# Optimization experiments

Hardware: AMD Instinct MI355X
Metric: run time of the kernel (lower is better)

Reference implementation:

```python
import jax, jax.numpy as jnp
import numpy as np

N = 1026; DX = 4096; DG = 4096; H0 = 4096; H1 = 2048; H2 = 1024
OUTS = 512; NL = 10; JH = 2048; E = 32832; K = 128; ALPHA = 0.05
INS = DX + DG  # 8192, edgeconv1 / joint_gemb input width

def _w(k, fan_in, shape):
    s = 1.0 / np.sqrt(fan_in)
    return jax.random.uniform(k, shape, minval=-s, maxval=s, dtype=jnp.float32)

def setup_inputs() -> dict:
    key = jax.random.key(0)
    ks = jax.random.split(key, 32)
    return dict(
        x=jax.random.normal(ks[0], (N, DX), jnp.float32),
        gx=jax.random.normal(ks[1], (N, DG), jnp.float32),
        edge_index=jax.random.randint(ks[2], (2, E), 0, N, dtype=jnp.int32),
        jw1=_w(ks[3], INS, (INS, JH)), jb1=_w(ks[4], INS, (JH,)),
        jw2=_w(ks[5], JH, (JH, N)), jb2=_w(ks[6], JH, (N,)),
        ec1_w=_w(ks[7], INS, (INS, H0)), ec1_b=_w(ks[8], INS, (H0,)),
        dr_w=_w(ks[9], H0, (H0, H2)), dr_b=_w(ks[10], H0, (H2,)),
        g1_w=_w(ks[11], H0, (H0, H1)), g1_b=_w(ks[12], H0, (H1,)),
        g2_w=_w(ks[13], H1, (H1, H2)), g2_b=_w(ks[14], H1, (H2,)),
        ec2_w=_w(ks[15], H2 + H1 + H0, (H2 + H1 + H0, H2)), ec2_b=_w(ks[16], H2 + H1 + H0, (H2,)),
        ec3_w=_w(ks[17], H2, (H2, OUTS)), ec3_b=_w(ks[18], H2, (OUTS,)),
        out_w=_w(ks[19], OUTS, (OUTS, NL)), out_b=_w(ks[20], OUTS, (NL,)),
    )

def _gdc(A):
    # GDC: self_loop_weight=1, sym norm in, exact PPR (alpha), topk(k, dim=0) sparsify, col norm out
    n = A.shape[0]
    eye = jnp.eye(n, dtype=A.dtype)
    A = A + eye  # self loops, weight 1
    deg = A.sum(axis=1)
    dinv = jax.lax.rsqrt(jnp.where(deg > 0, deg, 1.0))
    T = dinv[:, None] * A * dinv[None, :]          # D^-1/2 (A+I) D^-1/2
    S = ALPHA * jnp.linalg.inv(eye - (1.0 - ALPHA) * T)  # exact PPR diffusion
    vals, idx = jax.lax.top_k(S.T, K)              # top-K per column (dim=0)
    St = jnp.zeros((n, n), S.dtype).at[jnp.arange(n)[:, None], idx].set(vals)
    S = St.T
    csum = S.sum(axis=0)
    return S / jnp.where(csum == 0, 1.0, csum)[None, :]  # col normalization out

def _gcn(h_in, W, b, row, col, n):
    # PyG GCNConv: add self loops, sym-normalized aggregation, then bias
    h = h_in @ W
    deg = jax.ops.segment_sum(jnp.ones(row.shape[0], h.dtype), col, num_segments=n) + 1.0
    dinv = jax.lax.rsqrt(deg)
    agg = jax.ops.segment_sum(h[row] * (dinv[row] * dinv[col])[:, None], col, num_segments=n)
    return agg + h * (dinv * dinv)[:, None] + b

def _forward(x, gx, edge_index, jw1, jb1, jw2, jb2, ec1_w, ec1_b, dr_w, dr_b,
             g1_w, g1_b, g2_w, g2_b, ec2_w, ec2_b, ec3_w, ec3_b, out_w, out_b):
    row, col = edge_index[0], edge_index[1]
    xg = jnp.concatenate([x, gx], axis=1)                    # [N, INS]
    zz = jax.nn.relu(jax.nn.relu(xg @ jw1 + jb1) @ jw2 + jb2)  # joint_gemb -> [N, N] adjacency
    zz = _gdc(zz)
    xn = zz @ x                                              # nconv: dense neighbor aggregation
    z = jax.nn.relu(jnp.concatenate([xn, gx], axis=1) @ ec1_w + ec1_b)  # [N, H0]
    z0 = z @ dr_w + dr_b                                     # [N, H2]
    z1 = jax.nn.relu(_gcn(z + gx, g1_w, g1_b, row, col, N))  # [N, H1]
    z2 = jax.nn.relu(_gcn(z1, g2_w, g2_b, row, col, N))      # [N, H2]
    zc = jax.nn.relu(jnp.concatenate([z, z1, z2], axis=1) @ ec2_w + ec2_b)
    zf = jax.nn.relu((zc + z0) @ ec3_w + ec3_b)
    return zf @ out_w + out_b                                # [N, NL]

def reference(x, gx, edge_index, jw1, jb1, jw2, jb2, ec1_w, ec1_b, dr_w, dr_b,
              g1_w, g1_b, g2_w, g2_b, ec2_w, ec2_b, ec3_w, ec3_b, out_w, out_b):
    return _forward(x, gx, edge_index, jw1, jb1, jw2, jb2, ec1_w, ec1_b, dr_w, dr_b,
                    g1_w, g1_b, g2_w, g2_b, ec2_w, ec2_b, ec3_w, ec3_b, out_w, out_b)
```

## Files before the change

### kernel.cpp

```cpp
#include <hip/hip_runtime.h>
#include <stdint.h>

static constexpr int N_   = 1026;
static constexpr int DX_  = 4096;
static constexpr int DG_  = 4096;
static constexpr int H0_  = 4096;
static constexpr int H1_  = 2048;
static constexpr int H2_  = 1024;
static constexpr int OUTS_= 512;
static constexpr int NL_  = 10;
static constexpr int JH_  = 2048;
static constexpr int E_   = 32832;
static constexpr int K_   = 128;
static constexpr int INS_ = DX_ + DG_;
static constexpr int CAT2_= H0_ + H1_ + H2_;

static constexpr int MP_   = 1152;
static constexpr int KP1_  = 1056;

typedef _Float16 f16;
typedef __attribute__((ext_vector_type(8))) _Float16 f16x8;
typedef __attribute__((ext_vector_type(4))) _Float16 f16x4;
typedef __attribute__((ext_vector_type(4))) float    f32x4;

#define AS1C(p) ((const __attribute__((address_space(1))) unsigned int*)(p))
#define AS3(p)  ((__attribute__((address_space(3))) unsigned int*)(p))

__device__ __forceinline__ void gload16(const f16* g, f16* s) {
    __builtin_amdgcn_global_load_lds(AS1C(g), AS3(s), 16, 0, 0);
}

template<bool RELU, bool DUAL>
__global__ __launch_bounds__(512, DUAL ? 4 : 8)
void gemm_f16x2(int M, int Nc, int Kt, int chunkSteps,
                const f16* __restrict__ Ah, const f16* __restrict__ Al, int lda,
                const f16* __restrict__ Bh, const f16* __restrict__ Bl, int ldb,
                const float* __restrict__ bias, float alpha,
                const float* __restrict__ D, int ldd, float dscale,
                float* __restrict__ C, int ldc,
                f16* __restrict__ oAh, f16* __restrict__ oAl, int ldoa,
                f16* __restrict__ oBh, f16* __restrict__ oBl, int ldob,
                float* __restrict__ P, int Mp, int Ncp)
{
    __shared__ __align__(16) f16 sm[2][DUAL ? 4 : 2][4096];
    const int tid  = threadIdx.x;
    const int lane = tid & 63, w = tid >> 6;
    const int wr = w >> 1, wc = w & 1;
    const int bm = blockIdx.y * 128, bn = blockIdx.x * 128;
    const int z  = blockIdx.z;

    const int totalSteps = Kt >> 5;
    const int sBeg = z * chunkSteps;
    int nst = totalSteps - sBeg; if (nst > chunkSteps) nst = chunkSteps;

    const int srow  = w * 16 + (tid & 15);
    const int skoff = ((tid >> 4) & 3) * 8;
    const size_t arow = (size_t)(bm + srow) * lda + skoff;
    const size_t brow = (size_t)(bn + srow) * ldb + skoff;
    const int wslot = w * 512;
    const int fr = (lane >> 4) * 128 + (lane & 15) * 8;
    const int iaBase = wr * 1024 + fr;
    const int ibBase = wc * 2048 + fr;
    constexpr int PB = DUAL ? 8192 : 4096;

    f32x4 acc[2][4] = {};

    auto stage = [&](int buf, size_t ka) {
        f16* s0 = (f16*)&sm[buf][0][0];
        gload16(Ah + arow + ka, s0 + wslot);
        if constexpr (DUAL) gload16(Al + arow + ka, s0 + 4096 + wslot);
        gload16(Bh + brow + ka, s0 + PB + wslot);
        if constexpr (DUAL) gload16(Bl + brow + ka, s0 + PB + 4096 + wslot);
    };

    if (nst > 0) {
        const size_t kb = (size_t)sBeg * 32;
        stage(0, kb);
        for (int s = 0; s < nst; ++s) {
            if (s + 1 < nst) {
                stage((s + 1) & 1, kb + (size_t)(s + 1) * 32);
                if constexpr (DUAL)
                    asm volatile("s_waitcnt vmcnt(4)\n\ts_barrier" ::: "memory");
                else
                    asm volatile("s_waitcnt vmcnt(2)\n\ts_barrier" ::: "memory");
            } else {
                asm volatile("s_waitcnt vmcnt(0)\n\ts_barrier" ::: "memory");
            }
            const int b = s & 1;
            f16x8 ah[2], al[2], bh4[4], bl4[4];
            #pragma unroll
            for (int i = 0; i < 2; ++i) {
                ah[i] = *(const f16x8*)&sm[b][0][iaBase + i * 512];
                if constexpr (DUAL) al[i] = *(const f16x8*)&sm[b][1][iaBase + i * 512];
            }
            #pragma unroll
            for (int j = 0; j < 4; ++j) {
                bh4[j] = *(const f16x8*)&sm[b][DUAL ? 2 : 1][ibBase + j * 512];
                if constexpr (DUAL) bl4[j] = *(const f16x8*)&sm[b][3][ibBase + j * 512];
            }
            #pragma unroll
            for (int i = 0; i < 2; ++i)
                #pragma unroll
                for (int j = 0; j < 4; ++j) {
                    acc[i][j] = __builtin_amdgcn_mfma_f32_16x16x32_f16(ah[i], bh4[j], acc[i][j], 0, 0, 0);
                    if constexpr (DUAL) {
                        acc[i][j] = __builtin_amdgcn_mfma_f32_16x16x32_f16(ah[i], bl4[j], acc[i][j], 0, 0, 0);
                        acc[i][j] = __builtin_amdgcn_mfma_f32_16x16x32_f16(al[i], bh4[j], acc[i][j], 0, 0, 0);
                    }
                }
            if (s + 1 < nst) asm volatile("s_barrier" ::: "memory");
        }
    }

    const int er = (lane >> 4) * 4;
    const int ec = lane & 15;
    const int m00 = bm + wr * 32, n00 = bn + wc * 64;

    if (P) {
        float* Pz = P + (size_t)z * Mp * Ncp;
        #pragma unroll
        for (int mi = 0; mi < 2; ++mi)
            #pragma unroll
            for (int nj = 0; nj < 4; ++nj) {
                const int gc = n00 + nj * 16 + ec;
                const int gr = m00 + mi * 16 + er;
                float* p = Pz + (size_t)gr * Ncp + gc;
                f32x4 a = acc[mi][nj];
                #pragma unroll
                for (int r = 0; r < 4; ++r) p[(size_t)r * Ncp] = a[r];
            }
        return;
    }

    #pragma unroll
    for (int mi = 0; mi < 2; ++mi) {
        #pragma unroll
        for (int nj = 0; nj < 4; ++nj) {
            const int gcol = n00 + nj * 16 + ec;
            if (gcol >= Nc) continue;
            const float bv = bias ? bias[gcol] : 0.f;
            f32x4 a = acc[mi][nj];
            #pragma unroll
            for (int r = 0; r < 4; ++r) {
                const int grow = m00 + mi * 16 + er + r;
                if (grow >= M) continue;
                float val = alpha * a[r];
                if (D) val = fmaf(dscale, D[(size_t)grow * ldd + gcol], val);
                val += bv;
                if (RELU) val = fmaxf(val, 0.f);
                if (C) C[(size_t)grow * ldc + gcol] = val;
                if (oAh) {
                    f16 h = (f16)val, l = (f16)(val - (float)h);
                    oAh[(size_t)grow * ldoa + gcol] = h;
                    oAl[(size_t)grow * ldoa + gcol] = l;
                }
                if (oBh) {
                    f16 h = (f16)val, l = (f16)(val - (float)h);
                    oBh[(size_t)gcol * ldob + grow] = h;
                    oBl[(size_t)gcol * ldob + grow] = l;
                }
            }
        }
    }
}

template<bool RELU>
__global__ __launch_bounds__(256)
void combine_k(int M, int Nc, int nz, int Mp, int Ncp,
               const float* __restrict__ P,
               const float* __restrict__ bias, float alpha,
               const float* __restrict__ D, int ldd, float dscale,
               float* __restrict__ C, int ldc,
               f16* __restrict__ oAh, f16* __restrict__ oAl, int ldoa,
               f16* __restrict__ oBh, f16* __restrict__ oBl, int ldob)
{
    unsigned idx = blockIdx.x * 256 + threadIdx.x;
    if (idx >= (unsigned)(M * Nc)) return;
    int row = idx / (unsigned)Nc, col = idx - row * Nc;
    const float* p = P + (size_t)row * Ncp + col;
    float s = 0.f;
    for (int zz = 0; zz < nz; ++zz) s += p[(size_t)zz * Mp * Ncp];
    float val = alpha * s;
    if (D) val = fmaf(dscale, D[(size_t)row * ldd + col], val);
    if (bias) val += bias[col];
    if (RELU) val = fmaxf(val, 0.f);
    if (C) C[(size_t)row * ldc + col] = val;
    if (oAh) {
        f16 h = (f16)val, l = (f16)(val - (float)h);
        oAh[(size_t)row * ldoa + col] = h;
        oAl[(size_t)row * ldoa + col] = l;
    }
    if (oBh) {
        f16 h = (f16)val, l = (f16)(val - (float)h);
        oBh[(size_t)col * ldob + row] = h;
        oBl[(size_t)col * ldob + row] = l;
    }
}

__global__ __launch_bounds__(512, 4)
void pchain_k(int roleBase,
              const f16* __restrict__ uAh, const f16* __restrict__ uAl,
              const float* __restrict__ PfIn, float* __restrict__ PfOut,
              f16* __restrict__ oPh, f16* __restrict__ oPl,
              const f16* __restrict__ sAh, const f16* __restrict__ sAl,
              f16* __restrict__ oAh, f16* __restrict__ oAl,
              f16* __restrict__ oAth, f16* __restrict__ oAtl,
              const f16* __restrict__ Bh, const f16* __restrict__ Bl)
{
    __shared__ __align__(16) f16 sm[2][4][4096];
    const int tid  = threadIdx.x;
    const int lane = tid & 63, w = tid >> 6;
    const int wr = w >> 1, wc = w & 1;
    const int bm = blockIdx.y * 128, bn = blockIdx.x * 128;
    const int role = roleBase + blockIdx.z;
    const f16* Ah = (role == 0) ? uAh : sAh;
    const f16* Al = (role == 0) ? uAl : sAl;

    const int srow  = w * 16 + (tid & 15);
    const int skoff = ((tid >> 4) & 3) * 8;
    const size_t arow = (size_t)(bm + srow) * KP1_ + skoff;
    const size_t brow = (size_t)(bn + srow) * KP1_ + skoff;
    const int wslot = w * 512;
    const int fr = (lane >> 4) * 128 + (lane & 15) * 8;
    const int iaBase = wr * 1024 + fr;
    const int ibBase = wc * 2048 + fr;

    f32x4 acc[2][4] = {};

    auto stage = [&](int buf, size_t ka) {
        f16* s0 = (f16*)&sm[buf][0][0];
        gload16(Ah + arow + ka, s0 + wslot);
        gload16(Al + arow + ka, s0 + 4096 + wslot);
        gload16(Bh + brow + ka, s0 + 8192 + wslot);
        gload16(Bl + brow + ka, s0 + 12288 + wslot);
    };

    constexpr int nst = KP1_ / 32;
    stage(0, 0);
    for (int s = 0; s < nst; ++s) {
        if (s + 1 < nst) {
            stage((s + 1) & 1, (size_t)(s + 1) * 32);
            asm volatile("s_waitcnt vmcnt(4)\n\ts_barrier" ::: "memory");
        } else {
            asm volatile("s_waitcnt vmcnt(0)\n\ts_barrier" ::: "memory");
        }
        const int b = s & 1;
        f16x8 ah[2], al[2], bh4[4], bl4[4];
        #pragma unroll
        for (int i = 0; i < 2; ++i) {
            ah[i]  = *(const f16x8*)&sm[b][0][iaBase + i * 512];
            al[i]  = *(const f16x8*)&sm[b][1][iaBase + i * 512];
        }
        #pragma unroll
        for (int j = 0; j < 4; ++j) {
            bh4[j] = *(const f16x8*)&sm[b][2][ibBase + j * 512];
            bl4[j] = *(const f16x8*)&sm[b][3][ibBase + j * 512];
        }
        #pragma unroll
        for (int i = 0; i < 2; ++i)
            #pragma unroll
            for (int j = 0; j < 4; ++j) {
                acc[i][j] = __builtin_amdgcn_mfma_f32_16x16x32_f16(ah[i], bh4[j], acc[i][j], 0, 0, 0);
                acc[i][j] = __builtin_amdgcn_mfma_f32_16x16x32_f16(ah[i], bl4[j], acc[i][j], 0, 0, 0);
                acc[i][j] = __builtin_amdgcn_mfma_f32_16x16x32_f16(al[i], bh4[j], acc[i][j], 0, 0, 0);
            }
        if (s + 1 < nst) asm volatile("s_barrier" ::: "memory");
    }

    const int er = (lane >> 4) * 4;
    const int ec = lane & 15;
    const int m00 = bm + wr * 32, n00 = bn + wc * 64;
    #pragma unroll
    for (int mi = 0; mi < 2; ++mi) {
        #pragma unroll
        for (int nj = 0; nj < 4; ++nj) {
            const int gcol = n00 + nj * 16 + ec;
            if (gcol >= N_) continue;
            f32x4 a = acc[mi][nj];
            #pragma unroll
            for (int r = 0; r < 4; ++r) {
                const int grow = m00 + mi * 16 + er + r;
                if (grow >= N_) continue;
                if (role == 0) {
                    float val = a[r] + PfIn[(size_t)grow * N_ + gcol];
                    PfOut[(size_t)grow * N_ + gcol] = val;
                    if (oPh) {
                        f16 h = (f16)val, l = (f16)(val - (float)h);
                        oPh[(size_t)grow * KP1_ + gcol] = h;
                        oPl[(size_t)grow * KP1_ + gcol] = l;
                    }
                } else {
                    float val = a[r];
                    f16 h = (f16)val, l = (f16)(val - (float)h);
                    oAh[(size_t)grow * KP1_ + gcol] = h;
                    oAl[(size_t)grow * KP1_ + gcol] = l;
                    oAth[(size_t)gcol * KP1_ + grow] = h;
                    oAtl[(size_t)gcol * KP1_ + grow] = l;
                }
            }
        }
    }
}

__global__ void build_A_k(const float* __restrict__ zz, const float* __restrict__ dinv,
                          f16* __restrict__ aAh, f16* __restrict__ aAl,
                          f16* __restrict__ aBth, f16* __restrict__ aBtl,
                          float* __restrict__ Pf,
                          f16* __restrict__ pAh, f16* __restrict__ pAl)
{
    int idx = blockIdx.x * 256 + threadIdx.x;
    if (idx >= N_ * N_) return;
    int i = idx / N_, j = idx - i * N_;
    float diag = (i == j) ? 1.f : 0.f;
    float a = 0.95f * dinv[i] * (zz[idx] + diag) * dinv[j];
    f16 h = (f16)a, l = (f16)(a - (float)h);
    aAh[(size_t)i * KP1_ + j] = h;  aAl[(size_t)i * KP1_ + j] = l;
    aBth[(size_t)j * KP1_ + i] = h; aBtl[(size_t)j * KP1_ + i] = l;
    float p = a + diag;
    Pf[idx] = p;
    f16 ph = (f16)p, pl = (f16)(p - (float)ph);
    pAh[(size_t)i * KP1_ + j] = ph; pAl[(size_t)i * KP1_ + j] = pl;
}

__global__ void conv_A_k(const float* __restrict__ src, int R, int C, int lds,
                         f16* __restrict__ dh, f16* __restrict__ dl, int ldd,
                         int Rp, int Cp)
{
    size_t i4 = ((size_t)blockIdx.x * 256 + threadIdx.x) * 4;
    if (i4 >= (size_t)Rp * Cp) return;
    int r = (int)(i4 / Cp), c = (int)(i4 % Cp);
    float v[4] = {0.f, 0.f, 0.f, 0.f};
    if (r < R) {
        if (((lds & 3) == 0) && c + 3 < C) {
            float4 f = *(const float4*)&src[(size_t)r * lds + c];
            v[0] = f.x; v[1] = f.y; v[2] = f.z; v[3] = f.w;
        } else {
            #pragma unroll
            for (int q = 0; q < 4; ++q) v[q] = (c + q < C) ? src[(size_t)r * lds + c + q] : 0.f;
        }
    }
    f16x4 h, l;
    #pragma unroll
    for (int q = 0; q < 4; ++q) { h[q] = (f16)v[q]; l[q] = (f16)(v[q] - (float)h[q]); }
    *(f16x4*)&dh[(size_t)r * ldd + c] = h;
    *(f16x4*)&dl[(size_t)r * ldd + c] = l;
}

__global__ __launch_bounds__(256)
void conv_Bt_k(const float* __restrict__ src, int K, int N,
               f16* __restrict__ dh, f16* __restrict__ dl, int ldk,
               int Kp, int Np)
{
    __shared__ float t[32][65];
    const int bk = blockIdx.x * 32, bn = blockIdx.y * 64;
    const int tid = threadIdx.x;
    {
        const int kk = tid >> 4;
        const int nn = (tid & 15) * 4;
        #pragma unroll
        for (int p = 0; p < 2; ++p) {
            int k = bk + kk + p * 16;
            float v[4] = {0.f, 0.f, 0.f, 0.f};
            if (k < K) {
                int n = bn + nn;
                if (((N & 3) == 0) && n + 3 < N) {
                    float4 f = *(const float4*)&src[(size_t)k * N + n];
                    v[0] = f.x; v[1] = f.y; v[2] = f.z; v[3] = f.w;
                } else {
                    #pragma unroll
                    for (int q = 0; q < 4; ++q) v[q] = (n + q < N) ? src[(size_t)k * N + n + q] : 0.f;
                }
            }
            #pragma unroll
            for (int q = 0; q < 4; ++q) t[kk + p * 16][nn + q] = v[q];
        }
    }
    __syncthreads();
    {
        const int nn0 = tid >> 3;
        const int k4  = (tid & 7) * 4;
        #pragma unroll
        for (int p = 0; p < 2; ++p) {
            int n = bn + nn0 + p * 32;
            int k = bk + k4;
            if (n < Np && k < Kp) {
                f16x4 h, l;
                #pragma unroll
                for (int q = 0; q < 4; ++q) {
                    float vv = t[k4 + q][nn0 + p * 32];
                    h[q] = (f16)vv; l[q] = (f16)(vv - (float)h[q]);
                }
                *(f16x4*)&dh[(size_t)n * ldk + k] = h;
                *(f16x4*)&dl[(size_t)n * ldk + k] = l;
            }
        }
    }
}

__global__ void cat2_conv_k(const float* __restrict__ a, const float* __restrict__ b,
                            f16* __restrict__ dh, f16* __restrict__ dl)
{
    size_t i4 = ((size_t)blockIdx.x * 256 + threadIdx.x) * 4;
    if (i4 >= (size_t)MP_ * 8192) return;
    int r = (int)(i4 / 8192), c = (int)(i4 % 8192);
    float v[4] = {0.f, 0.f, 0.f, 0.f};
    if (r < N_) {
        const float* s = (c < 4096) ? &a[(size_t)r * 4096 + c] : &b[(size_t)r * 4096 + (c - 4096)];
        float4 f = *(const float4*)s;
        v[0] = f.x; v[1] = f.y; v[2] = f.z; v[3] = f.w;
    }
    f16x4 h, l;
    #pragma unroll
    for (int q = 0; q < 4; ++q) { h[q] = (f16)v[q]; l[q] = (f16)(v[q] - (float)h[q]); }
    *(f16x4*)&dh[i4] = h;
    *(f16x4*)&dl[i4] = l;
}

__global__ void zgx_conv_k(const f16* __restrict__ zh, const f16* __restrict__ zl,
                           const float* __restrict__ gx,
                           f16* __restrict__ dh, f16* __restrict__ dl)
{
    size_t i4 = ((size_t)blockIdx.x * 256 + threadIdx.x) * 4;
    if (i4 >= (size_t)MP_ * 4096) return;
    int r = (int)(i4 / 4096), c = (int)(i4 % 4096);
    f16x4 h = {}, l = {};
    if (r < N_) {
        f16x4 zh4 = *(const f16x4*)&zh[(size_t)r * CAT2_ + c];
        f16x4 zl4 = *(const f16x4*)&zl[(size_t)r * CAT2_ + c];
        float4 g4 = *(const float4*)&gx[(size_t)r * 4096 + c];
        float gv[4] = {g4.x, g4.y, g4.z, g4.w};
        #pragma unroll
        for (int q = 0; q < 4; ++q) {
            float v = (float)zh4[q] + (float)zl4[q] + gv[q];
            h[q] = (f16)v; l[q] = (f16)(v - (float)h[q]);
        }
    }
    *(f16x4*)&dh[i4] = h;
    *(f16x4*)&dl[i4] = l;
}

__global__ void zc_conv_k(const float* __restrict__ zc, const float* __restrict__ z0,
                          f16* __restrict__ dh, f16* __restrict__ dl)
{
    size_t i4 = ((size_t)blockIdx.x * 256 + threadIdx.x) * 4;
    if (i4 >= (size_t)MP_ * 1024) return;
    int r = (int)(i4 / 1024), c = (int)(i4 % 1024);
    f16x4 h = {}, l = {};
    if (r < N_) {
        float4 a4 = *(const float4*)&zc[(size_t)r * 1024 + c];
        float4 b4 = *(const float4*)&z0[(size_t)r * 1024 + c];
        float av[4] = {a4.x, a4.y, a4.z, a4.w};
        float bv[4] = {b4.x, b4.y, b4.z, b4.w};
        #pragma unroll
        for (int q = 0; q < 4; ++q) {
            float v = av[q] + bv[q];
            h[q] = (f16)v; l[q] = (f16)(v - (float)h[q]);
        }
    }
    *(f16x4*)&dh[i4] = h;
    *(f16x4*)&dl[i4] = l;
}

template<int NPARTS, bool RELU>
__global__ __launch_bounds__(256)
void gemm_k(int M, int Nc, int Kt,
            const float* __restrict__ A0, int w0,
            const float* __restrict__ A1, int w1,
            const float* __restrict__ A2, int w2,
            const float* __restrict__ B, int ldb,
            const float* __restrict__ bias,
            float alpha, const float* __restrict__ D, float dscale,
            float* __restrict__ C, int ldc)
{
    __shared__ __align__(16) float As[16][68];
    __shared__ __align__(16) float Bs[16][68];
    const int tid = threadIdx.x;
    const int tx = tid & 15, ty = tid >> 4;
    const int bm = blockIdx.y * 64, bn = blockIdx.x * 64;
    const int w01 = w0 + w1;
    float acc[4][4] = {};

    for (int kt = 0; kt < Kt; kt += 16) {
        #pragma unroll
        for (int r = 0; r < 4; ++r) {
            int idx = tid + r * 256;
            int m = idx >> 4, kk = idx & 15;
            int row = bm + m, k = kt + kk;
            float v = 0.f;
            if (row < M && k < Kt) {
                if (NPARTS == 1) v = A0[(size_t)row * w0 + k];
                else {
                    if (k < w0) v = A0[(size_t)row * w0 + k];
                    else if (NPARTS == 2 || k < w01) v = A1[(size_t)row * w1 + (k - w0)];
                    else v = A2[(size_t)row * w2 + (k - w01)];
                }
            }
            As[kk][m] = v;
        }
        #pragma unroll
        for (int r = 0; r < 4; ++r) {
            int idx = tid + r * 256;
            int kk = idx >> 6, nn = idx & 63;
            int k = kt + kk, c = bn + nn;
            Bs[kk][nn] = (k < Kt && c < Nc) ? B[(size_t)k * ldb + c] : 0.f;
        }
        __syncthreads();
        #pragma unroll
        for (int kk = 0; kk < 16; ++kk) {
            float4 a4 = *(const float4*)&As[kk][ty * 4];
            float4 b4 = *(const float4*)&Bs[kk][tx * 4];
            float av[4] = {a4.x, a4.y, a4.z, a4.w};
            float bv[4] = {b4.x, b4.y, b4.z, b4.w};
            #pragma unroll
            for (int i = 0; i < 4; ++i)
                #pragma unroll
                for (int j = 0; j < 4; ++j)
                    acc[i][j] = fmaf(av[i], bv[j], acc[i][j]);
        }
        __syncthreads();
    }

    #pragma unroll
    for (int i = 0; i < 4; ++i) {
        int row = bm + ty * 4 + i;
        if (row >= M) continue;
        #pragma unroll
        for (int j = 0; j < 4; ++j) {
            int col = bn + tx * 4 + j;
            if (col >= Nc) continue;
            float val = alpha * acc[i][j];
            if (D)    val += dscale * D[(size_t)row * ldc + col];
            if (bias) val += bias[col];
            if (RELU) val = fmaxf(val, 0.f);
            C[(size_t)row * ldc + col] = val;
        }
    }
}

__global__ void row_dinv_k(const float* __restrict__ zz, float* __restrict__ dinv) {
    __shared__ float red[256];
    int i = blockIdx.x, t = threadIdx.x;
    float s = 0.f;
    for (int j = t; j < N_; j += 256) s += zz[(size_t)i * N_ + j];
    red[t] = s; __syncthreads();
    for (int k = 128; k > 0; k >>= 1) { if (t < k) red[t] += red[t + k]; __syncthreads(); }
    if (t == 0) dinv[i] = 1.0f / sqrtf(red[0] + 1.0f);
}

__global__ void build_MX_k(const float* __restrict__ zz, const float* __restrict__ dinv,
                           float* __restrict__ Mm, float* __restrict__ X) {
    int idx = blockIdx.x * 256 + threadIdx.x;
    if (idx >= N_ * N_) return;
    int i = idx / N_, j = idx - i * N_;
    float diag = (i == j) ? 1.f : 0.f;
    float t = dinv[i] * (zz[idx] + diag) * dinv[j];
    float m = diag - 0.95f * t;
    Mm[idx] = m;
    X[idx]  = 2.f * diag - m;
}

__global__ __launch_bounds__(256) void topk_colnorm_k(const float* __restrict__ X, float* __restrict__ S) {
    __shared__ float v[N_];
    __shared__ float svals[K_];
    __shared__ int   sidx[K_];
    __shared__ float wv[4];
    __shared__ int   wi[4];
    const int j = blockIdx.x, t = threadIdx.x;
    const int lane = t & 63, wid = t >> 6;
    for (int i = t; i < N_; i += 256) v[i] = X[(size_t)i * N_ + j];
    __syncthreads();
    for (int r = 0; r < K_; ++r) {
        float bv = -INFINITY; int bi = N_;
        for (int i = t; i < N_; i += 256) {
            float x = v[i];
            if (x > bv || (x == bv && i < bi)) { bv = x; bi = i; }
        }
        #pragma unroll
        for (int s = 32; s > 0; s >>= 1) {
            float ov = __shfl_xor(bv, s);
            int   oi = __shfl_xor(bi, s);
            if (ov > bv || (ov == bv && oi < bi)) { bv = ov; bi = oi; }
        }
        if (lane == 0) { wv[wid] = bv; wi[wid] = bi; }
        __syncthreads();
        float fv = wv[0]; int fi = wi[0];
        #pragma unroll
        for (int q = 1; q < 4; ++q) {
            float ov = wv[q]; int oi = wi[q];
            if (ov > fv || (ov == fv && oi < fi)) { fv = ov; fi = oi; }
        }
        if (t == 0) { svals[r] = fv; sidx[r] = fi; v[fi] = -INFINITY; }
        __syncthreads();
    }
    float s = (t < K_) ? svals[t] : 0.f;
    #pragma unroll
    for (int q = 32; q > 0; q >>= 1) s += __shfl_xor(s, q);
    if (lane == 0) wv[wid] = s;
    __syncthreads();
    float cs = wv[0] + wv[1] + wv[2] + wv[3];
    if (cs == 0.f) cs = 1.f;
    if (t < K_) S[(size_t)sidx[t] * N_ + j] = svals[t] / cs;
}

__global__ void add_k(const float* __restrict__ a, const float* __restrict__ b,
                      float* __restrict__ c, int n) {
    int i = blockIdx.x * 256 + threadIdx.x;
    if (i < n) c[i] = a[i] + b[i];
}
__global__ void fill_k(float* __restrict__ p, float v, int n) {
    int i = blockIdx.x * 256 + threadIdx.x;
    if (i < n) p[i] = v;
}
__global__ void edge_deg_k(const int* __restrict__ ei, float* __restrict__ deg) {
    int e = blockIdx.x * 256 + threadIdx.x;
    if (e < E_) atomicAdd(&deg[ei[E_ + e]], 1.0f);
}
__global__ void rsqrt_k(float* __restrict__ d, int n) {
    int i = blockIdx.x * 256 + threadIdx.x;
    if (i < n) d[i] = 1.0f / sqrtf(d[i]);
}
__global__ void edge_G_k(const int* __restrict__ ei, const float* __restrict__ dinv,
                         float* __restrict__ G) {
    int e = blockIdx.x * 256 + threadIdx.x;
    if (e < E_) {
        int r = ei[e], c = ei[E_ + e];
        atomicAdd(&G[(size_t)c * N_ + r], dinv[r] * dinv[c]);
    }
}
__global__ void diag_G_k(float* __restrict__ G, const float* __restrict__ dinv) {
    int i = blockIdx.x * 256 + threadIdx.x;
    if (i < N_) G[(size_t)i * N_ + i] += dinv[i] * dinv[i];
}

__global__ __launch_bounds__(1024) void deg_dinv_k(const int* __restrict__ ei,
                                                   float* __restrict__ dinv2) {
    __shared__ float deg[N_];
    int t = threadIdx.x;
    for (int i = t; i < N_; i += 1024) deg[i] = 1.f;
    __syncthreads();
    for (int e = t; e < E_; e += 1024) atomicAdd(&deg[ei[E_ + e]], 1.f);
    __syncthreads();
    for (int i = t; i < N_; i += 1024) dinv2[i] = 1.f / sqrtf(deg[i]);
}
__global__ void edge_diag_G_k(const int* __restrict__ ei, const float* __restrict__ dinv,
                              float* __restrict__ G) {
    int e = blockIdx.x * 256 + threadIdx.x;
    if (e < E_) {
        int r = ei[e], c = ei[E_ + e];
        atomicAdd(&G[(size_t)c * N_ + r], dinv[r] * dinv[c]);
    } else {
        int i = e - E_;
        if (i < N_) atomicAdd(&G[(size_t)i * N_ + i], dinv[i] * dinv[i]);
    }
}

struct HL { f16* h; f16* l; };
static const HL HL0 = {nullptr, nullptr};

static inline void g16(hipStream_t st, bool relu, bool dual, int M, int Nc, int Kt, int split,
                       HL A, int lda, HL B, int ldb,
                       const float* bias, float alpha,
                       const float* D, int ldd, float dscale,
                       float* C, int ldc,
                       HL oA, int ldoa, HL oB, int ldob, float* P)
{
    const int gx = (Nc + 127) / 128, gy = (M + 127) / 128;
    const int totalSteps = Kt >> 5;
    const int chunk = (totalSteps + split - 1) / split;
    const int Mp = gy * 128, Ncp = gx * 128;
    dim3 grid(gx, gy, split), blk(512);
    float* Pp = (split > 1) ? P : nullptr;
#define CALL_G16(RL, DU) gemm_f16x2<RL, DU><<<grid, blk, 0, st>>>(M, Nc, Kt, chunk, \
        A.h, A.l, lda, B.h, B.l, ldb, bias, alpha, D, ldd, dscale, C, ldc, \
        oA.h, oA.l, ldoa, oB.h, oB.l, ldob, Pp, Mp, Ncp)
    if (relu) { if (dual) CALL_G16(true, true); else CALL_G16(true, false); }
    else      { if (dual) CALL_G16(false, true); else CALL_G16(false, false); }
#undef CALL_G16
    if (split > 1) {
        unsigned tot = (unsigned)(M * Nc);
        dim3 cg((tot + 255) / 256);
        if (relu)
            combine_k<true><<<cg, 256, 0, st>>>(M, Nc, split, Mp, Ncp, P, bias, alpha,
                D, ldd, dscale, C, ldc, oA.h, oA.l, ldoa, oB.h, oB.l, ldob);
        else
            combine_k<false><<<cg, 256, 0, st>>>(M, Nc, split, Mp, Ncp, P, bias, alpha,
                D, ldd, dscale, C, ldc, oA.h, oA.l, ldoa, oB.h, oB.l, ldob);
    }
}

static inline void convA(hipStream_t st, const float* src, int R, int C, int lds,
                         HL d, int ldd, int Rp, int Cp)
{
    size_t total4 = (size_t)Rp * Cp / 4;
    conv_A_k<<<(int)((total4 + 255) / 256), 256, 0, st>>>(src, R, C, lds, d.h, d.l, ldd, Rp, Cp);
}
static inline void convBt(hipStream_t st, const float* src, int K, int N,
                          HL d, int ldk, int Kp, int Np)
{
    dim3 grid((Kp + 31) / 32, (Np + 63) / 64), blk(256);
    conv_Bt_k<<<grid, blk, 0, st>>>(src, K, N, d.h, d.l, ldk, Kp, Np);
}

static inline void launch_gemm_f32(hipStream_t st, bool relu, int nparts,
                                   int M, int Nc, int Kt,
                                   const float* A0, int w0, const float* A1, int w1,
                                   const float* A2, int w2,
                                   const float* B, int ldb, const float* bias,
                                   float alpha, const float* D, float dscale,
                                   float* C, int ldc)
{
    dim3 g((Nc + 63) / 64, (M + 63) / 64), b(256);
#define CALL_GEMM(NP, RL) gemm_k<NP, RL><<<g, b, 0, st>>>(M, Nc, Kt, A0, w0, A1, w1, A2, w2, B, ldb, bias, alpha, D, dscale, C, ldc)
    if (relu) { if (nparts == 1) CALL_GEMM(1, true); else if (nparts == 2) CALL_GEMM(2, true); else CALL_GEMM(3, true); }
    else      { if (nparts == 1) CALL_GEMM(1, false); else if (nparts == 2) CALL_GEMM(2, false); else CALL_GEMM(3, false); }
#undef CALL_GEMM
}

static constexpr size_t catA1_e = (size_t)MP_ * 8192;
static constexpr size_t jw1Bt_e = (size_t)2048 * 8192;
static constexpr size_t jw2Bt_e = (size_t)MP_ * 2048;
static constexpr size_t h1A_e   = (size_t)MP_ * 2048;
static constexpr size_t nb_e    = (size_t)MP_ * KP1_;
static constexpr size_t ec1Bt_e = (size_t)4096 * 8192;
static constexpr size_t drBt_e  = (size_t)1024 * 4096;
static constexpr size_t g1Bt_e  = (size_t)2048 * 4096;
static constexpr size_t g2Bt_e  = (size_t)1024 * 2048;
static constexpr size_t ec2Bt_e = (size_t)1024 * 7168;
static constexpr size_t ec3Bt_e = (size_t)512 * 1024;
static constexpr size_t hg1Bt_e = (size_t)2048 * KP1_;
static constexpr size_t hg2Bt_e = (size_t)1024 * KP1_;
static constexpr size_t catA2_e = (size_t)MP_ * 8192;
static constexpr size_t SA_e    = nb_e;
static constexpr size_t GA_e    = nb_e;
static constexpr size_t xBt_e   = (size_t)4096 * KP1_;
static constexpr size_t zgxA_e  = (size_t)MP_ * 4096;
static constexpr size_t cat3_e  = (size_t)MP_ * 7168;
static constexpr size_t zcA_e   = (size_t)MP_ * 1024;

static constexpr size_t u_catA1 = 0;
static constexpr size_t u_jw1Bt = u_catA1 + 2 * catA1_e;
static constexpr size_t u_jw2Bt = u_jw1Bt + 2 * jw1Bt_e;
static constexpr size_t u_h1A   = u_jw2Bt + 2 * jw2Bt_e;
static constexpr size_t u_nb0   = u_h1A + 2 * h1A_e;
static constexpr size_t u_nb1   = u_nb0 + 2 * nb_e;
static constexpr size_t u_nb2   = u_nb1 + 2 * nb_e;
static constexpr size_t u_nb3   = u_nb2 + 2 * nb_e;
static constexpr size_t u_nb4   = u_nb3 + 2 * nb_e;
static constexpr size_t u_nb5   = u_nb4 + 2 * nb_e;
static constexpr size_t UNION_F16 = u_nb5 + 2 * nb_e;
static_assert(2 * ec1Bt_e <= UNION_F16, "ec1Bt alias");
static constexpr size_t u_drBt  = 0;
static constexpr size_t u_g1Bt  = u_drBt + 2 * drBt_e;
static constexpr size_t u_g2Bt  = u_g1Bt + 2 * g1Bt_e;
static constexpr size_t u_ec2Bt = u_g2Bt + 2 * g2Bt_e;
static constexpr size_t u_ec3Bt = u_ec2Bt + 2 * ec2Bt_e;
static constexpr size_t u_hg1Bt = u_ec3Bt + 2 * ec3Bt_e;
static constexpr size_t u_hg2Bt = u_hg1Bt + 2 * hg1Bt_e;
static_assert(u_hg2Bt + 2 * hg2Bt_e <= UNION_F16, "phase3 alias");

static constexpr size_t o_catA2 = 0;
static constexpr size_t o_SA    = o_catA2 + 2 * catA2_e;
static constexpr size_t o_GA    = o_SA + 2 * SA_e;
static constexpr size_t o_xBt   = o_GA + 2 * GA_e;
static constexpr size_t o_zgxA  = o_xBt + 2 * xBt_e;
static constexpr size_t o_cat3  = o_zgxA + 2 * zgxA_e;
static constexpr size_t o_zcA   = o_cat3 + 2 * cat3_e;
static constexpr size_t OUT_F16 = o_zcA + 2 * zcA_e;

static constexpr size_t NN_     = (size_t)N_ * N_;
static constexpr size_t F16_TOTAL = UNION_F16 + OUT_F16;
static constexpr size_t f_zz = 0, f_Mm = NN_, f_X0 = 2 * NN_, f_X1 = 3 * NN_,
                        f_S = 4 * NN_, f_G = 5 * NN_, f_z0 = 6 * NN_,
                        f_zc = f_z0 + (size_t)N_ * 1024,
                        f_zf = f_zc + (size_t)N_ * 1024,
                        f_dinv = f_zf + (size_t)N_ * 512,
                        f_dinv2 = f_dinv + 1028,
                        F32_TOTAL = f_dinv2 + 1028;
static constexpr size_t P_e = (size_t)2 * MP_ * 4096;
static constexpr size_t FAST_WS_BYTES = F16_TOTAL * 2 + (F32_TOTAL + P_e) * 4;

static void run_fast(void* const* d_in, float* out, void* d_ws, hipStream_t st)
{
    const float* x    = (const float*)d_in[0];
    const float* gx   = (const float*)d_in[1];
    const int*   ei   = (const int*)d_in[2];
    const float* jw1  = (const float*)d_in[3];
    const float* jb1  = (const float*)d_in[4];
    const float* jw2  = (const float*)d_in[5];
    const float* jb2  = (const float*)d_in[6];
    const float* ec1w = (const float*)d_in[7];
    const float* ec1b = (const float*)d_in[8];
    const float* drw  = (const float*)d_in[9];
    const float* drb  = (const float*)d_in[10];
    const float* g1w  = (const float*)d_in[11];
    const float* g1b  = (const float*)d_in[12];
    const float* g2w  = (const float*)d_in[13];
    const float* g2b  = (const float*)d_in[14];
    const float* ec2w = (const float*)d_in[15];
    const float* ec2b = (const float*)d_in[16];
    const float* ec3w = (const float*)d_in[17];
    const float* ec3b = (const float*)d_in[18];
    const float* outw = (const float*)d_in[19];
    const float* outb = (const float*)d_in[20];

    f16*   fb   = (f16*)d_ws;
    float* f32b = (float*)((char*)d_ws + F16_TOTAL * 2);
    float* P    = f32b + F32_TOTAL;

    auto mk = [&](size_t off, size_t elems) { return HL{fb + off, fb + off + elems}; };
    HL catA1 = mk(u_catA1, catA1_e), jw1Bt = mk(u_jw1Bt, jw1Bt_e),
       jw2Bt = mk(u_jw2Bt, jw2Bt_e), h1A = mk(u_h1A, h1A_e);
    HL pA[2]  = {mk(u_nb0, nb_e), mk(u_nb1, nb_e)};
    HL aA[2]  = {mk(u_nb2, nb_e), mk(u_nb3, nb_e)};
    HL aBt[2] = {mk(u_nb4, nb_e), mk(u_nb5, nb_e)};
    HL ec1Bt = mk(0, ec1Bt_e);
    HL drBt = mk(u_drBt, drBt_e), g1Bt = mk(u_g1Bt, g1Bt_e), g2Bt = mk(u_g2Bt, g2Bt_e),
       ec2Bt = mk(u_ec2Bt, ec2Bt_e), ec3Bt = mk(u_ec3Bt, ec3Bt_e),
       hg1Bt = mk(u_hg1Bt, hg1Bt_e), hg2Bt = mk(u_hg2Bt, hg2Bt_e);
    HL catA2 = mk(UNION_F16 + o_catA2, catA2_e), SA = mk(UNION_F16 + o_SA, SA_e),
       GA = mk(UNION_F16 + o_GA, GA_e), xBt = mk(UNION_F16 + o_xBt, xBt_e),
       zgxA = mk(UNION_F16 + o_zgxA, zgxA_e), cat3 = mk(UNION_F16 + o_cat3, cat3_e),
       zcA = mk(UNION_F16 + o_zcA, zcA_e);
    float *zz = f32b + f_zz, *Pf[2] = {f32b + f_X0, f32b + f_X1},
          *S = f32b + f_S, *G = f32b + f_G, *z0 = f32b + f_z0, *zc = f32b + f_zc,
          *zf = f32b + f_zf, *dinv = f32b + f_dinv, *dinv2 = f32b + f_dinv2;

    hipMemsetAsync(fb + u_nb0, 0, (UNION_F16 - u_nb0) * sizeof(f16), st);

    {
        size_t t4 = (size_t)MP_ * 8192 / 4;
        cat2_conv_k<<<(int)((t4 + 255) / 256), 256, 0, st>>>(x, gx, catA1.h, catA1.l);
    }
    convBt(st, jw1, 8192, 2048, jw1Bt, 8192, 8192, 2048);
    g16(st, true, true, 1026, 2048, 8192, 4, catA1, 8192, jw1Bt, 8192, jb1, 1.f,
        nullptr, 0, 0.f, nullptr, 0, h1A, 2048, HL0, 0, P);
    convBt(st, jw2, 2048, 1026, jw2Bt, 2048, 2048, MP_);
    g16(st, true, true, 1026, 1026, 2048, 7, h1A, 2048, jw2Bt, 2048, jb2, 1.f,
        nullptr, 0, 0.f, zz, 1026, HL0, 0, HL0, 0, P);
    row_dinv_k<<<N_, 256, 0, st>>>(zz, dinv);
    build_A_k<<<(int)((NN_ + 255) / 256), 256, 0, st>>>(zz, dinv,
        aA[0].h, aA[0].l, aBt[0].h, aBt[0].l, Pf[0], pA[0].h, pA[0].l);
    pchain_k<<<dim3(9, 9, 1), 512, 0, st>>>(1,
        nullptr, nullptr, nullptr, nullptr, nullptr, nullptr,
        aA[0].h, aA[0].l, aA[1].h, aA[1].l, aBt[1].h, aBt[1].l,
        aBt[0].h, aBt[0].l);
    int ac = 1, pc = 0;
    for (int k = 2; k <= 8; ++k) {
        pchain_k<<<dim3(9, 9, 2), 512, 0, st>>>(0,
            pA[pc].h, pA[pc].l, Pf[pc], Pf[1 - pc], pA[1 - pc].h, pA[1 - pc].l,
            aA[ac].h, aA[ac].l, aA[1 - ac].h, aA[1 - ac].l, aBt[1 - ac].h, aBt[1 - ac].l,
            aBt[ac].h, aBt[ac].l);
        pc ^= 1; ac ^= 1;
    }
    pchain_k<<<dim3(9, 9, 1), 512, 0, st>>>(0,
        pA[pc].h, pA[pc].l, Pf[pc], Pf[1 - pc], nullptr, nullptr,
        nullptr, nullptr, nullptr, nullptr, nullptr, nullptr,
        aBt[ac].h, aBt[ac].l);
    float* Xfin = Pf[1 - pc];
    hipMemsetAsync(S, 0, NN_ * sizeof(float), st);
    topk_colnorm_k<<<N_, 256, 0, st>>>(Xfin, S);
    convA(st, S, N_, N_, N_, SA, KP1_, MP_, KP1_);
    convBt(st, x, 1026, 4096, xBt, KP1_, KP1_, 4096);
    g16(st, false, true, 1026, 4096, KP1_, 2, SA, KP1_, xBt, KP1_, nullptr, 1.f,
        nullptr, 0, 0.f, nullptr, 0, HL{catA2.h, catA2.l}, 8192, HL0, 0, P);
    convA(st, gx, N_, 4096, 4096, HL{catA2.h + 4096, catA2.l + 4096}, 8192, MP_, 4096);
    convBt(st, ec1w, 8192, 4096, ec1Bt, 8192, 8192, 4096);
    g16(st, true, false, 1026, 4096, 8192, 2, catA2, 8192, ec1Bt, 8192, ec1b, 1.f,
        nullptr, 0, 0.f, nullptr, 0, HL{cat3.h, cat3.l}, 7168, HL0, 0, P);
    deg_dinv_k<<<1, 1024, 0, st>>>(ei, dinv2);
    hipMemsetAsync(G, 0, NN_ * sizeof(float), st);
    edge_diag_G_k<<<(E_ + N_ + 255) / 256, 256, 0, st>>>(ei, dinv2, G);
    convA(st, G, N_, N_, N_, GA, KP1_, MP_, KP1_);
    convBt(st, drw, 4096, 1024, drBt, 4096, 4096, 1024);
    g16(st, false, false, 1026, 1024, 4096, 8, HL{cat3.h, cat3.l}, 7168, drBt, 4096, drb, 1.f,
        nullptr, 0, 0.f, z0, 1024, HL0, 0, HL0, 0, P);
    {
        size_t t4 = (size_t)MP_ * 4096 / 4;
        zgx_conv_k<<<(int)((t4 + 255) / 256), 256, 0, st>>>(cat3.h, cat3.l, gx, zgxA.h, zgxA.l);
    }
    convBt(st, g1w, 4096, 2048, g1Bt, 4096, 4096, 2048);
    hipMemsetAsync(fb + u_hg1Bt, 0, (2 * hg1Bt_e + 2 * hg2Bt_e) * sizeof(f16), st);
    g16(st, false, false, 2048, 1026, 4096, 4, g1Bt, 4096, zgxA, 4096, nullptr, 1.f,
        nullptr, 0, 0.f, nullptr, 0, hg1Bt, KP1_, HL0, 0, P);
    g16(st, true, false, 1026, 2048, KP1_, 4, GA, KP1_, hg1Bt, KP1_, g1b, 1.f,
        nullptr, 0, 0.f, nullptr, 0, HL{cat3.h + 4096, cat3.l + 4096}, 7168, HL0, 0, P);
    convBt(st, g2w, 2048, 1024, g2Bt, 2048, 2048, 1024);
    g16(st, false, false, 1024, 1026, 2048, 8, g2Bt, 2048, HL{cat3.h + 4096, cat3.l + 4096}, 7168,
        nullptr, 1.f, nullptr, 0, 0.f, nullptr, 0, hg2Bt, KP1_, HL0, 0, P);
    g16(st, true, false, 1026, 1024, KP1_, 8, GA, KP1_, hg2Bt, KP1_, g2b, 1.f,
        nullptr, 0, 0.f, nullptr, 0, HL{cat3.h + 6144, cat3.l + 6144}, 7168, HL0, 0, P);
    convBt(st, ec2w, 7168, 1024, ec2Bt, 7168, 7168, 1024);
    g16(st, true, false, 1026, 1024, 7168, 8, cat3, 7168, ec2Bt, 7168, ec2b, 1.f,
        nullptr, 0, 0.f, zc, 1024, HL0, 0, HL0, 0, P);
    {
        size_t t4 = (size_t)MP_ * 1024 / 4;
        zc_conv_k<<<(int)((t4 + 255) / 256), 256, 0, st>>>(zc, z0, zcA.h, zcA.l);
    }
    convBt(st, ec3w, 1024, 512, ec3Bt, 1024, 1024, 512);
    g16(st, true, false, 1026, 512, 1024, 8, zcA, 1024, ec3Bt, 1024, ec3b, 1.f,
        nullptr, 0, 0.f, zf, 512, HL0, 0, HL0, 0, P);
    launch_gemm_f32(st, false, 1, N_, NL_, OUTS_, zf, OUTS_, nullptr, 0, nullptr, 0,
                    outw, NL_, outb, 1.f, nullptr, 0.f, out, NL_);
}

static void run_ref(void* const* d_in, float* out, void* d_ws, hipStream_t stream)
{
    const float* x    = (const float*)d_in[0];
    const float* gx   = (const float*)d_in[1];
    const int*   ei   = (const int*)d_in[2];
    const float* jw1  = (const float*)d_in[3];
    const float* jb1  = (const float*)d_in[4];
    const float* jw2  = (const float*)d_in[5];
    const float* jb2  = (const float*)d_in[6];
    const float* ec1w = (const float*)d_in[7];
    const float* ec1b = (const float*)d_in[8];
    const float* drw  = (const float*)d_in[9];
    const float* drb  = (const float*)d_in[10];
    const float* g1w  = (const float*)d_in[11];
    const float* g1b  = (const float*)d_in[12];
    const float* g2w  = (const float*)d_in[13];
    const float* g2b  = (const float*)d_in[14];
    const float* ec2w = (const float*)d_in[15];
    const float* ec2b = (const float*)d_in[16];
    const float* ec3w = (const float*)d_in[17];
    const float* ec3b = (const float*)d_in[18];
    const float* outw = (const float*)d_in[19];
    const float* outb = (const float*)d_in[20];

    float* ws = (float*)d_ws;
    size_t off = 0;
    float* H1buf = ws + off; off += (size_t)N_ * JH_;
    float* ZZ    = ws + off; off += NN_;
    float* Mm    = ws + off; off += NN_;
    float* Xa    = ws + off; off += NN_;
    float* Xb    = ws + off; off += NN_;
    float* S     = ws + off; off += NN_;
    float* G     = ws + off; off += NN_;
    float* dinv  = ws + off; off += 1028;
    float* dinv2 = ws + off; off += 1028;
    float* XN    = ws + off; off += (size_t)N_ * H0_;
    float* Z     = ws + off; off += (size_t)N_ * H0_;
    float* ZGX   = ws + off; off += (size_t)N_ * H0_;
    float* Z0    = ws + off; off += (size_t)N_ * H2_;
    float* HG1   = ws + off; off += (size_t)N_ * H1_;
    float* Z1    = ws + off; off += (size_t)N_ * H1_;
    float* HG2   = ws + off; off += (size_t)N_ * H2_;
    float* Z2    = ws + off; off += (size_t)N_ * H2_;
    float* ZC    = ws + off; off += (size_t)N_ * H2_;
    float* ZF    = ws + off; off += (size_t)N_ * OUTS_;

    launch_gemm_f32(stream, true, 2, N_, JH_, INS_, x, DX_, gx, DG_, nullptr, 0,
                    jw1, JH_, jb1, 1.f, nullptr, 0.f, H1buf, JH_);
    launch_gemm_f32(stream, true, 1, N_, N_, JH_, H1buf, JH_, nullptr, 0, nullptr, 0,
                    jw2, N_, jb2, 1.f, nullptr, 0.f, ZZ, N_);
    row_dinv_k<<<N_, 256, 0, stream>>>(ZZ, dinv);
    build_MX_k<<<(int)((NN_ + 255) / 256), 256, 0, stream>>>(ZZ, dinv, Mm, Xa);
    float* Xcur = Xa; float* Xalt = Xb; float* W = H1buf;
    for (int it = 0; it < 9; ++it) {
        launch_gemm_f32(stream, false, 1, N_, N_, N_, Mm, N_, nullptr, 0, nullptr, 0,
                        Xcur, N_, nullptr, 1.f, nullptr, 0.f, W, N_);
        launch_gemm_f32(stream, false, 1, N_, N_, N_, Xcur, N_, nullptr, 0, nullptr, 0,
                        W, N_, nullptr, -1.f, Xcur, 2.f, Xalt, N_);
        float* tmp = Xcur; Xcur = Xalt; Xalt = tmp;
    }
    hipMemsetAsync(S, 0, NN_ * sizeof(float), stream);
    topk_colnorm_k<<<N_, 256, 0, stream>>>(Xcur, S);
    launch_gemm_f32(stream, false, 1, N_, DX_, N_, S, N_, nullptr, 0, nullptr, 0,
                    x, DX_, nullptr, 1.f, nullptr, 0.f, XN, DX_);
    launch_gemm_f32(stream, true, 2, N_, H0_, INS_, XN, DX_, gx, DG_, nullptr, 0,
                    ec1w, H0_, ec1b, 1.f, nullptr, 0.f, Z, H0_);
    launch_gemm_f32(stream, false, 1, N_, H2_, H0_, Z, H0_, nullptr, 0, nullptr, 0,
                    drw, H2_, drb, 1.f, nullptr, 0.f, Z0, H2_);
    add_k<<<(int)(((size_t)N_ * H0_ + 255) / 256), 256, 0, stream>>>(Z, gx, ZGX, N_ * H0_);
    fill_k<<<(N_ + 255) / 256, 256, 0, stream>>>(dinv2, 1.0f, N_);
    edge_deg_k<<<(E_ + 255) / 256, 256, 0, stream>>>(ei, dinv2);
    rsqrt_k<<<(N_ + 255) / 256, 256, 0, stream>>>(dinv2, N_);
    hipMemsetAsync(G, 0, NN_ * sizeof(float), stream);
    edge_G_k<<<(E_ + 255) / 256, 256, 0, stream>>>(ei, dinv2, G);
    diag_G_k<<<(N_ + 255) / 256, 256, 0, stream>>>(G, dinv2);
    launch_gemm_f32(stream, false, 1, N_, H1_, H0_, ZGX, H0_, nullptr, 0, nullptr, 0,
                    g1w, H1_, nullptr, 1.f, nullptr, 0.f, HG1, H1_);
    launch_gemm_f32(stream, true, 1, N_, H1_, N_, G, N_, nullptr, 0, nullptr, 0,
                    HG1, H1_, g1b, 1.f, nullptr, 0.f, Z1, H1_);
    launch_gemm_f32(stream, false, 1, N_, H2_, H1_, Z1, H1_, nullptr, 0, nullptr, 0,
                    g2w, H2_, nullptr, 1.f, nullptr, 0.f, HG2, H2_);
    launch_gemm_f32(stream, true, 1, N_, H2_, N_, G, N_, nullptr, 0, nullptr, 0,
                    HG2, H2_, g2b, 1.f, nullptr, 0.f, Z2, H2_);
    launch_gemm_f32(stream, true, 3, N_, H2_, CAT2_, Z, H0_, Z1, H1_, Z2, H2_,
                    ec2w, H2_, ec2b, 1.f, nullptr, 0.f, ZC, H2_);
    add_k<<<(int)(((size_t)N_ * H2_ + 255) / 256), 256, 0, stream>>>(ZC, Z0, ZC, N_ * H2_);
    launch_gemm_f32(stream, true, 1, N_, OUTS_, H2_, ZC, H2_, nullptr, 0, nullptr, 0,
                    ec3w, OUTS_, ec3b, 1.f, nullptr, 0.f, ZF, OUTS_);
    launch_gemm_f32(stream, false, 1, N_, NL_, OUTS_, ZF, OUTS_, nullptr, 0, nullptr, 0,
                    outw, NL_, outb, 1.f, nullptr, 0.f, out, NL_);
}

extern "C" void kernel_launch(void* const* d_in, const int* in_sizes, int n_in,
                              void* d_out, int out_size, void* d_ws, size_t ws_size,
                              hipStream_t stream)
{
    (void)in_sizes; (void)n_in; (void)out_size;
    if (ws_size >= FAST_WS_BYTES + 4096)
        run_fast(d_in, (float*)d_out, d_ws, stream);
    else
        run_ref(d_in, (float*)d_out, d_ws, stream);
}
```

Measured before the change: 1.744 ms.

## Split-K the PPR power-chain GEMMs with a combine kernel; bitonic top-k sort

```diff
diff --git a/kernel.cpp b/kernel.cpp
--- a/kernel.cpp
+++ b/kernel.cpp
@@ -198,23 +198,25 @@
 }
 
 __global__ __launch_bounds__(512, 4)
-void pchain_k(int roleBase,
+void pchain_k(int roleBase, int split, int chunkSteps,
               const f16* __restrict__ uAh, const f16* __restrict__ uAl,
-              const float* __restrict__ PfIn, float* __restrict__ PfOut,
-              f16* __restrict__ oPh, f16* __restrict__ oPl,
               const f16* __restrict__ sAh, const f16* __restrict__ sAl,
-              f16* __restrict__ oAh, f16* __restrict__ oAl,
-              f16* __restrict__ oAth, f16* __restrict__ oAtl,
-              const f16* __restrict__ Bh, const f16* __restrict__ Bl)
+              const f16* __restrict__ Bh, const f16* __restrict__ Bl,
+              float* __restrict__ Pp)
 {
     __shared__ __align__(16) f16 sm[2][4][4096];
     const int tid  = threadIdx.x;
     const int lane = tid & 63, w = tid >> 6;
     const int wr = w >> 1, wc = w & 1;
     const int bm = blockIdx.y * 128, bn = blockIdx.x * 128;
-    const int role = roleBase + blockIdx.z;
+    const int z = blockIdx.z;
+    const int role = roleBase + z / split;
+    const int sub  = z % split;
     const f16* Ah = (role == 0) ? uAh : sAh;
     const f16* Al = (role == 0) ? uAl : sAl;
+
+    const int sBeg = sub * chunkSteps;
+    int nst = KP1_ / 32 - sBeg; if (nst > chunkSteps) nst = chunkSteps;
 
     const int srow  = w * 16 + (tid & 15);
     const int skoff = ((tid >> 4) & 3) * 8;
@@ -235,11 +237,11 @@
         gload16(Bl + brow + ka, s0 + 12288 + wslot);
     };
 
-    constexpr int nst = KP1_ / 32;
-    stage(0, 0);
+    const size_t kb = (size_t)sBeg * 32;
+    stage(0, kb);
     for (int s = 0; s < nst; ++s) {
         if (s + 1 < nst) {
-            stage((s + 1) & 1, (size_t)(s + 1) * 32);
+            stage((s + 1) & 1, kb + (size_t)(s + 1) * 32);
             asm volatile("s_waitcnt vmcnt(4)\n\ts_barrier" ::: "memory");
         } else {
             asm volatile("s_waitcnt vmcnt(0)\n\ts_barrier" ::: "memory");
@@ -267,38 +269,56 @@
         if (s + 1 < nst) asm volatile("s_barrier" ::: "memory");
     }
 
+    float* Pz = Pp + (size_t)z * (1152 * 1152);
     const int er = (lane >> 4) * 4;
     const int ec = lane & 15;
     const int m00 = bm + wr * 32, n00 = bn + wc * 64;
     #pragma unroll
-    for (int mi = 0; mi < 2; ++mi) {
+    for (int mi = 0; mi < 2; ++mi)
         #pragma unroll
         for (int nj = 0; nj < 4; ++nj) {
-            const int gcol = n00 + nj * 16 + ec;
-            if (gcol >= N_) continue;
+            const int gc = n00 + nj * 16 + ec;
+            const int gr = m00 + mi * 16 + er;
+            float* p = Pz + (size_t)gr * 1152 + gc;
             f32x4 a = acc[mi][nj];
             #pragma unroll
-            for (int r = 0; r < 4; ++r) {
-                const int grow = m00 + mi * 16 + er + r;
-                if (grow >= N_) continue;
-                if (role == 0) {
-                    float val = a[r] + PfIn[(size_t)grow * N_ + gcol];
-                    PfOut[(size_t)grow * N_ + gcol] = val;
-                    if (oPh) {
-                        f16 h = (f16)val, l = (f16)(val - (float)h);
-                        oPh[(size_t)grow * KP1_ + gcol] = h;
-                        oPl[(size_t)grow * KP1_ + gcol] = l;
-                    }
-                } else {
-                    float val = a[r];
-                    f16 h = (f16)val, l = (f16)(val - (float)h);
-                    oAh[(size_t)grow * KP1_ + gcol] = h;
-                    oAl[(size_t)grow * KP1_ + gcol] = l;
-                    oAth[(size_t)gcol * KP1_ + grow] = h;
-                    oAtl[(size_t)gcol * KP1_ + grow] = l;
-                }
-            }
-        }
+            for (int r = 0; r < 4; ++r) p[(size_t)r * 1152] = a[r];
+        }
+}
+
+__global__ __launch_bounds__(256)
+void pchain_combine_k(int nz, int hasUpd, int hasSq, const float* __restrict__ Pp,
+                      const float* __restrict__ PfIn, float* __restrict__ PfOut,
+                      f16* __restrict__ oPh, f16* __restrict__ oPl,
+                      float* __restrict__ XT,
+                      f16* __restrict__ oAh, f16* __restrict__ oAl,
+                      f16* __restrict__ oAth, f16* __restrict__ oAtl)
+{
+    unsigned idx = blockIdx.x * 256 + threadIdx.x;
+    if (idx >= (unsigned)(N_ * N_)) return;
+    int row = idx / (unsigned)N_, col = idx - row * N_;
+    const size_t zs = (size_t)1152 * 1152;
+    const size_t poff = (size_t)row * 1152 + col;
+    int zb = 0;
+    if (hasUpd) {
+        float s = 0.f;
+        for (int z = 0; z < nz; ++z) s += Pp[(size_t)(zb + z) * zs + poff];
+        float val = s + PfIn[idx];
+        PfOut[idx] = val;
+        if (oPh) {
+            f16 h = (f16)val, l = (f16)(val - (float)h);
+            oPh[(size_t)row * KP1_ + col] = h;
+            oPl[(size_t)row * KP1_ + col] = l;
+        }
+        if (XT) XT[(size_t)col * N_ + row] = val;
+        zb += nz;
+    }
+    if (hasSq) {
+        float s = 0.f;
+        for (int z = 0; z < nz; ++z) s += Pp[(size_t)(zb + z) * zs + poff];
+        f16 h = (f16)s, l = (f16)(s - (float)h);
+        oAh[(size_t)row * KP1_ + col] = h;  oAl[(size_t)row * KP1_ + col] = l;
+        oAth[(size_t)col * KP1_ + row] = h; oAtl[(size_t)col * KP1_ + row] = l;
     }
 }
 
@@ -320,6 +340,56 @@
     Pf[idx] = p;
     f16 ph = (f16)p, pl = (f16)(p - (float)ph);
     pAh[(size_t)i * KP1_ + j] = ph; pAl[(size_t)i * KP1_ + j] = pl;
+}
+
+__global__ __launch_bounds__(256)
+void topk_sort_k(const float* __restrict__ XT, float* __restrict__ S)
+{
+    __shared__ uint64_t key[2048];
+    __shared__ float red[4];
+    const int j = blockIdx.x, t = threadIdx.x;
+    for (int i = t; i < 2048; i += 256) {
+        uint64_t kk;
+        if (i < N_) {
+            float v = XT[(size_t)j * N_ + i];
+            unsigned u = __float_as_uint(v);
+            unsigned sv = (u & 0x80000000u) ? ~u : (u | 0x80000000u);
+            kk = ((uint64_t)(~sv) << 32) | (unsigned)i;
+        } else kk = ~0ULL;
+        key[i] = kk;
+    }
+    __syncthreads();
+    for (int k = 2; k <= 2048; k <<= 1) {
+        for (int jj = k >> 1; jj > 0; jj >>= 1) {
+            #pragma unroll
+            for (int q = 0; q < 8; ++q) {
+                int i = t + q * 256;
+                int ixj = i ^ jj;
+                if (ixj > i) {
+                    uint64_t a = key[i], b = key[ixj];
+                    bool up = ((i & k) == 0);
+                    if ((a > b) == up) { key[i] = b; key[ixj] = a; }
+                }
+            }
+            __syncthreads();
+        }
+    }
+    float val = 0.f; int idx = 0;
+    if (t < K_) {
+        uint64_t kk = key[t];
+        unsigned sv = ~(unsigned)(kk >> 32);
+        unsigned u = (sv & 0x80000000u) ? (sv & 0x7FFFFFFFu) : ~sv;
+        val = __uint_as_float(u);
+        idx = (int)(kk & 0xFFFFFFFFu);
+    }
+    float sm = (t < K_) ? val : 0.f;
+    #pragma unroll
+    for (int q = 32; q > 0; q >>= 1) sm += __shfl_xor(sm, q);
+    if ((t & 63) == 0) red[t >> 6] = sm;
+    __syncthreads();
+    float cs = red[0] + red[1] + red[2] + red[3];
+    if (cs == 0.f) cs = 1.f;
+    if (t < K_) S[(size_t)idx * N_ + j] = val / cs;
 }
 
 __global__ void conv_A_k(const float* __restrict__ src, int R, int C, int lds,
@@ -778,6 +848,7 @@
                         F32_TOTAL = f_dinv2 + 1028;
 static constexpr size_t P_e = (size_t)2 * MP_ * 4096;
 static constexpr size_t FAST_WS_BYTES = F16_TOTAL * 2 + (F32_TOTAL + P_e) * 4;
+static_assert((size_t)6 * 1152 * 1152 <= P_e, "pchain partial fit");
 
 static void run_fast(void* const* d_in, float* out, void* d_ws, hipStream_t st)
 {
@@ -821,7 +892,7 @@
        GA = mk(UNION_F16 + o_GA, GA_e), xBt = mk(UNION_F16 + o_xBt, xBt_e),
        zgxA = mk(UNION_F16 + o_zgxA, zgxA_e), cat3 = mk(UNION_F16 + o_cat3, cat3_e),
        zcA = mk(UNION_F16 + o_zcA, zcA_e);
-    float *zz = f32b + f_zz, *Pf[2] = {f32b + f_X0, f32b + f_X1},
+    float *zz = f32b + f_zz, *XT = f32b + f_Mm, *Pf[2] = {f32b + f_X0, f32b + f_X1},
           *S = f32b + f_S, *G = f32b + f_G, *z0 = f32b + f_z0, *zc = f32b + f_zc,
           *zf = f32b + f_zf, *dinv = f32b + f_dinv, *dinv2 = f32b + f_dinv2;
 
@@ -840,25 +911,31 @@
     row_dinv_k<<<N_, 256, 0, st>>>(zz, dinv);
     build_A_k<<<(int)((NN_ + 255) / 256), 256, 0, st>>>(zz, dinv,
         aA[0].h, aA[0].l, aBt[0].h, aBt[0].l, Pf[0], pA[0].h, pA[0].l);
-    pchain_k<<<dim3(9, 9, 1), 512, 0, st>>>(1,
-        nullptr, nullptr, nullptr, nullptr, nullptr, nullptr,
-        aA[0].h, aA[0].l, aA[1].h, aA[1].l, aBt[1].h, aBt[1].l,
-        aBt[0].h, aBt[0].l);
-    int ac = 1, pc = 0;
-    for (int k = 2; k <= 8; ++k) {
-        pchain_k<<<dim3(9, 9, 2), 512, 0, st>>>(0,
-            pA[pc].h, pA[pc].l, Pf[pc], Pf[1 - pc], pA[1 - pc].h, pA[1 - pc].l,
-            aA[ac].h, aA[ac].l, aA[1 - ac].h, aA[1 - ac].l, aBt[1 - ac].h, aBt[1 - ac].l,
-            aBt[ac].h, aBt[ac].l);
-        pc ^= 1; ac ^= 1;
-    }
-    pchain_k<<<dim3(9, 9, 1), 512, 0, st>>>(0,
-        pA[pc].h, pA[pc].l, Pf[pc], Pf[1 - pc], nullptr, nullptr,
-        nullptr, nullptr, nullptr, nullptr, nullptr, nullptr,
-        aBt[ac].h, aBt[ac].l);
-    float* Xfin = Pf[1 - pc];
+    {
+        const int PS = 3, PCH = 11;
+        dim3 cg((unsigned)((NN_ + 255) / 256));
+        pchain_k<<<dim3(9, 9, PS), 512, 0, st>>>(1, PS, PCH,
+            nullptr, nullptr, aA[0].h, aA[0].l, aBt[0].h, aBt[0].l, P);
+        pchain_combine_k<<<cg, 256, 0, st>>>(PS, 0, 1, P,
+            nullptr, nullptr, nullptr, nullptr, nullptr,
+            aA[1].h, aA[1].l, aBt[1].h, aBt[1].l);
+        int ac = 1, pc = 0;
+        for (int k = 2; k <= 8; ++k) {
+            pchain_k<<<dim3(9, 9, 2 * PS), 512, 0, st>>>(0, PS, PCH,
+                pA[pc].h, pA[pc].l, aA[ac].h, aA[ac].l, aBt[ac].h, aBt[ac].l, P);
+            pchain_combine_k<<<cg, 256, 0, st>>>(PS, 1, 1, P,
+                Pf[pc], Pf[1 - pc], pA[1 - pc].h, pA[1 - pc].l, nullptr,
+                aA[1 - ac].h, aA[1 - ac].l, aBt[1 - ac].h, aBt[1 - ac].l);
+            pc ^= 1; ac ^= 1;
+        }
+        pchain_k<<<dim3(9, 9, PS), 512, 0, st>>>(0, PS, PCH,
+            pA[pc].h, pA[pc].l, nullptr, nullptr, aBt[ac].h, aBt[ac].l, P);
+        pchain_combine_k<<<cg, 256, 0, st>>>(PS, 1, 0, P,
+            Pf[pc], Pf[1 - pc], nullptr, nullptr, XT,
+            nullptr, nullptr, nullptr, nullptr);
+    }
     hipMemsetAsync(S, 0, NN_ * sizeof(float), st);
-    topk_colnorm_k<<<N_, 256, 0, st>>>(Xfin, S);
+    topk_sort_k<<<N_, 256, 0, st>>>(XT, S);
     convA(st, S, N_, N_, N_, SA, KP1_, MP_, KP1_);
     convBt(st, x, 1026, 4096, xBt, KP1_, KP1_, 4096);
     g16(st, false, true, 1026, 4096, KP1_, 2, SA, KP1_, xBt, KP1_, nullptr, 1.f,
```

New measurement: 1.618 ms. -7.2%, faster.
